# Kernel optimization log

Hardware: AMD Instinct MI355X
Metric: run time of the kernel (lower is better)

Reference implementation:

```python
import jax, jax.numpy as jnp
import numpy as np

# config
HIDDEN = 1024
NUM_EXPERTS = 16
TOP_K = 4
MOE_INTER = 512
NUM_SHARED = 2
SHARED_INTER = MOE_INTER * NUM_SHARED  # 1024
NORM_TOPK = True
ROUTED_SCALE = 1.0
NUM_TOKENS = 1024


def setup_inputs() -> dict:
    key = jax.random.key(0)
    ks = jax.random.split(key, 8)
    s = 0.02
    return {
        "hidden_states": jax.random.normal(ks[0], (NUM_TOKENS, HIDDEN), jnp.float32),
        # router (BailingMoEGate): weight [E, H], no bias
        "router_w": jax.random.normal(ks[1], (NUM_EXPERTS, HIDDEN), jnp.float32) * s,
        # routed experts: gate/up proj [E, H, I], down proj [E, I, H]
        "w_gate": jax.random.normal(ks[2], (NUM_EXPERTS, HIDDEN, MOE_INTER), jnp.float32) * s,
        "w_up": jax.random.normal(ks[3], (NUM_EXPERTS, HIDDEN, MOE_INTER), jnp.float32) * s,
        "w_down": jax.random.normal(ks[4], (NUM_EXPERTS, MOE_INTER, HIDDEN), jnp.float32) * s,
        # shared experts (BailingMoEMLP, merged gate_up): [H, 2*Is], [Is, H]
        "ws_gate_up": jax.random.normal(ks[5], (HIDDEN, 2 * SHARED_INTER), jnp.float32) * s,
        "ws_down": jax.random.normal(ks[6], (SHARED_INTER, HIDDEN), jnp.float32) * s,
    }


def _moe_forward(x, router_w, w_gate, w_up, w_down, ws_gate_up, ws_down):
    T = x.shape[0]
    # ---- router: logits -> softmax -> top-k (score_function='softmax', no bias)
    logits = jnp.einsum("th,eh->te", x, router_w)          # [T, E]
    probs = jax.nn.softmax(logits, axis=-1)
    topk_w, topk_idx = jax.lax.top_k(probs, TOP_K)         # [T, K]
    if NORM_TOPK:
        topk_w = topk_w / jnp.sum(topk_w, axis=-1, keepdims=True)
    topk_w = topk_w * ROUTED_SCALE
    # sparse combine weights [T, E] (zeros for non-selected experts)
    combine = jnp.zeros((T, NUM_EXPERTS), x.dtype).at[
        jnp.arange(T)[:, None], topk_idx
    ].set(topk_w.astype(x.dtype))
    # ---- routed experts: SiLU(x W_gate) * (x W_up) then W_down, weighted combine
    g = jnp.einsum("th,ehi->tei", x, w_gate)               # [T, E, I]
    u = jnp.einsum("th,ehi->tei", x, w_up)
    h = jax.nn.silu(g) * u
    routed = jnp.einsum("tei,eih,te->th", h, w_down, combine)
    # ---- shared experts (dense SwiGLU MLP)
    gu = x @ ws_gate_up                                    # [T, 2*Is]
    g_s, u_s = jnp.split(gu, 2, axis=-1)
    shared = (jax.nn.silu(g_s) * u_s) @ ws_down
    return routed + shared


def reference(hidden_states, router_w, w_gate, w_up, w_down, ws_gate_up, ws_down):
    return _moe_forward(hidden_states, router_w, w_gate, w_up, w_down,
                        ws_gate_up, ws_down)
```

## Files before the change

### kernel.cpp

```cpp
#include <hip/hip_runtime.h>
#include <stdint.h>


typedef __attribute__((ext_vector_type(8))) unsigned short ushort8;
typedef __attribute__((ext_vector_type(4))) float f32x4;
typedef __attribute__((ext_vector_type(8))) __bf16 bf16x8;

#define T_TOK 1024
#define HID   1024
#define NEXP  16
#define TOPK  4
#define MINTER 512
#define SINTER 1024

constexpr size_t WGU_E = 32 * 1024 * 32;
constexpr size_t WD_E  = 16 * 1024 * 32;

constexpr size_t OFF_COUNTS = 0;
constexpr size_t OFF_LIST   = 1024;
constexpr size_t OFF_WT     = OFF_LIST  + 65536;
constexpr size_t OFF_TIDX   = OFF_WT    + 65536;
constexpr size_t OFF_XB     = OFF_TIDX  + 65536;
constexpr size_t OFF_HR     = OFF_XB    + 2097152;
constexpr size_t OFF_HS     = OFF_HR    + 4194304;
constexpr size_t OFF_WGU    = OFF_HS    + 2097152;
constexpr size_t OFF_WD     = OFF_WGU   + 33554432;
constexpr size_t OFF_WSGU   = OFF_WD    + 16777216;
constexpr size_t OFF_WSD    = OFF_WSGU  + 4194304;
constexpr size_t OFF_ROUT   = OFF_WGU;

__device__ __forceinline__ unsigned short f2bf(float f) {
  union { float f; uint32_t u; } v; v.f = f;
  uint32_t r = (v.u + 0x7FFFu + ((v.u >> 16) & 1u)) >> 16;
  return (unsigned short)r;
}
__device__ __forceinline__ float bfu2f(uint32_t u) {
  union { uint32_t u; float f; } v; v.u = u << 16; return v.f;
}
__device__ __forceinline__ bf16x8 as_bf16x8(ushort8 s) {
  union { ushort8 s; bf16x8 b; } u; u.s = s; return u.b;
}
__device__ __forceinline__ float silu(float g) { return g / (1.f + __expf(-g)); }

__device__ __forceinline__ void glds16(const unsigned short* g, unsigned short* l) {
  __builtin_amdgcn_global_load_lds(
      (const __attribute__((address_space(1))) unsigned int*)g,
      (__attribute__((address_space(3))) unsigned int*)l, 16, 0, 0);
}

#define PIPE_BARRIER4() asm volatile("s_waitcnt vmcnt(4) lgkmcnt(0)\ns_barrier" ::: "memory")
#define PIPE_BARRIER0() asm volatile("s_waitcnt vmcnt(0) lgkmcnt(0)\ns_barrier" ::: "memory")

__global__ void init_kernel(int* counts) {
  if (threadIdx.x < NEXP) counts[threadIdx.x] = 0;
}

__global__ __launch_bounds__(64) void router_kernel(
    const float* __restrict__ x, const float* __restrict__ rw,
    int* counts, int* list, float* wt, int* tIdx,
    unsigned short* __restrict__ Xb) {
  const int t = blockIdx.x, l = threadIdx.x;
  float xv[16];
#pragma unroll
  for (int j = 0; j < 16; j++) xv[j] = x[t * HID + j * 64 + l];
#pragma unroll
  for (int j = 0; j < 16; j++) Xb[t * HID + j * 64 + l] = f2bf(xv[j]);
  float p[NEXP];
#pragma unroll
  for (int e = 0; e < NEXP; e++) {
    float s = 0.f;
#pragma unroll
    for (int j = 0; j < 16; j++) s += xv[j] * rw[e * HID + j * 64 + l];
#pragma unroll
    for (int off = 32; off > 0; off >>= 1) s += __shfl_xor(s, off);
    p[e] = s;
  }
  float mx = p[0];
#pragma unroll
  for (int e = 1; e < NEXP; e++) mx = fmaxf(mx, p[e]);
  int idx[TOPK]; float w4[TOPK]; float wsum = 0.f; unsigned used = 0u;
#pragma unroll
  for (int k = 0; k < TOPK; k++) {
    float bv = -1e30f; int bi = 0;
#pragma unroll
    for (int e = 0; e < NEXP; e++)
      if (!((used >> e) & 1u) && p[e] > bv) { bv = p[e]; bi = e; }
    used |= 1u << bi;
    idx[k] = bi;
    w4[k] = __expf(p[bi] - mx);
    wsum += w4[k];
  }
  const float inv = 1.f / wsum;
  if (l < TOPK) {
    const int e = idx[l];
    const int pos = atomicAdd(&counts[e], 1);
    list[e * 1024 + pos] = t;
    wt[e * 1024 + pos]   = w4[l] * inv;
    tIdx[t * TOPK + l]   = (e << 10) | pos;
  }
}

__global__ __launch_bounds__(256) void pack_all_kernel(
    const float* __restrict__ Wg, const float* __restrict__ Wu,
    const float* __restrict__ Wd, const float* __restrict__ Wsgu,
    const float* __restrict__ Wsd,
    unsigned short* __restrict__ WGUp, unsigned short* __restrict__ WDp,
    unsigned short* __restrict__ WSGUp, unsigned short* __restrict__ WSDp) {
  const int bid = blockIdx.x;
  const float* src; unsigned short* dst; int C, Nj, kp0, r0, c0, jbase, ilv;
  if (bid < 2048) {
    const int e = bid >> 7, loc = bid & 127, kt = loc >> 3, nt = loc & 7;
    src = Wg + (size_t)e * HID * MINTER; dst = WGUp + (size_t)e * WGU_E;
    C = MINTER; Nj = 1024; kp0 = 2 * kt; r0 = 64 * kt; c0 = 64 * nt;
    jbase = 128 * nt; ilv = 1;
  } else if (bid < 4096) {
    const int e = (bid - 2048) >> 7, loc = bid & 127, kt = loc >> 3, nt = loc & 7;
    src = Wu + (size_t)e * HID * MINTER; dst = WGUp + (size_t)e * WGU_E;
    C = MINTER; Nj = 1024; kp0 = 2 * kt; r0 = 64 * kt; c0 = 64 * nt;
    jbase = 128 * nt + 16; ilv = 1;
  } else if (bid < 6144) {
    const int e = (bid - 4096) >> 7, loc = bid & 127, kt = loc >> 4, nt = loc & 15;
    src = Wd + (size_t)e * MINTER * HID; dst = WDp + (size_t)e * WD_E;
    C = HID; Nj = 1024; kp0 = 2 * kt; r0 = 64 * kt; c0 = 64 * nt;
    jbase = 64 * nt; ilv = 0;
  } else if (bid < 6656) {
    const int loc = bid - 6144, kt = loc >> 5, nt = loc & 31;
    src = Wsgu; dst = WSGUp;
    C = 2048; Nj = 2048; kp0 = 2 * kt; r0 = 64 * kt; c0 = 64 * nt;
    const int isU = (nt >= 16), ntc = nt & 15;
    jbase = 128 * ntc + 16 * isU; ilv = 1;
  } else {
    const int loc = bid - 6656, kt = loc >> 4, nt = loc & 15;
    src = Wsd; dst = WSDp;
    C = HID; Nj = 1024; kp0 = 2 * kt; r0 = 64 * kt; c0 = 64 * nt;
    jbase = 64 * nt; ilv = 0;
  }
  __shared__ float tile[64][65];
  const int t = threadIdx.x;
  {
    const int r = t >> 4, c4 = (t & 15) * 4;
#pragma unroll
    for (int p = 0; p < 4; p++) {
      const int rr = p * 16 + r;
      const float4 v = *(const float4*)(src + (size_t)(r0 + rr) * C + c0 + c4);
      tile[rr][c4 + 0] = v.x; tile[rr][c4 + 1] = v.y;
      tile[rr][c4 + 2] = v.z; tile[rr][c4 + 3] = v.w;
    }
  }
  __syncthreads();
  {
    const int n = t >> 2, k8 = (t & 3) * 8;
    const int j = jbase + (ilv ? (32 * (n >> 4) + (n & 15)) : n);
#pragma unroll
    for (int h = 0; h < 2; h++) {
      const int k = 32 * h + k8;
      union { unsigned short u[8]; ushort8 v; } pk;
#pragma unroll
      for (int i = 0; i < 8; i++) pk.u[i] = f2bf(tile[k + i][n]);
      *(ushort8*)(dst + ((size_t)(kp0 + h) * Nj + j) * 32 + k8) = pk.v;
    }
  }
}

__global__ __launch_bounds__(256, 3) void phase1_kernel(
    const unsigned short* __restrict__ Xb,
    const unsigned short* __restrict__ WGUp,
    const unsigned short* __restrict__ WSGUp,
    const int* __restrict__ counts, const int* __restrict__ list,
    const float* __restrict__ wt,
    unsigned short* __restrict__ Hr,
    unsigned short* __restrict__ Hs) {
  const int z = blockIdx.z, x = blockIdx.x, y = blockIdx.y;
  const bool routed = (z < NEXP);
  int cnt = 0, base = 0;
  if (routed) {
    if (x >= 8) return;
    cnt = counts[z];
    if (y * 128 >= cnt) return;
#pragma unroll
    for (int i = 0; i < NEXP; i++) base += (i < z) ? counts[i] : 0;
  }
  __shared__ __align__(16) unsigned short sA[3][128 * 32];
  __shared__ __align__(16) unsigned short sB[3][128 * 32];
  const int tid = threadIdx.x, w = tid >> 6, l = tid & 63;
  const int wm = w >> 1, wn = w & 1, m0 = y * 128;
  const int swz = ((l & 3) ^ ((l >> 3) & 3)) * 8;
  const int Nj = routed ? 1024 : 2048;

  const unsigned short* aS[2];
#pragma unroll
  for (int ii = 0; ii < 2; ii++) {
    const int r = 32 * w + 16 * ii + (l >> 2);
    const unsigned short* row = routed
        ? Xb + (size_t)list[z * 1024 + min(m0 + r, cnt - 1)] * HID
        : Xb + (size_t)(m0 + r) * HID;
    aS[ii] = row + swz;
  }
  const unsigned short* pan = routed ? WGUp + (size_t)z * WGU_E : WSGUp;
  const unsigned short* bS[2];
#pragma unroll
  for (int ii = 0; ii < 2; ii++)
    bS[ii] = pan + ((size_t)(x * 128 + 32 * w + 16 * ii + (l >> 2))) * 32 + swz;
  const size_t bStep = (size_t)Nj * 32;

  const int rsw = ((l >> 4) ^ (((l & 15) >> 1) & 3)) * 8;
  int aOff[4], bOff[4];
#pragma unroll
  for (int i = 0; i < 4; i++) aOff[i] = (64 * wm + 16 * i + (l & 15)) * 32 + rsw;
#pragma unroll
  for (int jt = 0; jt < 4; jt++) bOff[jt] = (64 * wn + 16 * jt + (l & 15)) * 32 + rsw;

  f32x4 acc[4][4];
#pragma unroll
  for (int i = 0; i < 4; i++)
#pragma unroll
    for (int jt = 0; jt < 4; jt++) acc[i][jt] = (f32x4){0.f, 0.f, 0.f, 0.f};

  auto stage = [&](int s, int b) {
    glds16(aS[0] + s * 32, &sA[b][(32 * w) * 32]);
    glds16(aS[1] + s * 32, &sA[b][(32 * w + 16) * 32]);
    glds16(bS[0] + s * bStep, &sB[b][(32 * w) * 32]);
    glds16(bS[1] + s * bStep, &sB[b][(32 * w + 16) * 32]);
  };

  const int steps = HID / 32;
  stage(0, 0); stage(1, 1);
#pragma unroll 1
  for (int s = 0; s < steps; s++) {
    const int cb = s % 3;
    if (s + 2 < steps)      { PIPE_BARRIER4(); stage(s + 2, (s + 2) % 3); }
    else if (s + 1 < steps) { PIPE_BARRIER4(); }
    else                    { PIPE_BARRIER0(); }
    const unsigned short* A = &sA[cb][0];
    const unsigned short* B = &sB[cb][0];
    bf16x8 af[4], bfr[4];
#pragma unroll
    for (int i = 0; i < 4; i++) af[i] = as_bf16x8(*(const ushort8*)(A + aOff[i]));
#pragma unroll
    for (int jt = 0; jt < 4; jt++) bfr[jt] = as_bf16x8(*(const ushort8*)(B + bOff[jt]));
#pragma unroll
    for (int jt = 0; jt < 4; jt++)
#pragma unroll
      for (int i = 0; i < 4; i++)
        acc[i][jt] = __builtin_amdgcn_mfma_f32_16x16x32_bf16(af[i], bfr[jt], acc[i][jt], 0, 0, 0);
  }

  const int rl = (l >> 4) * 4, cl = l & 15;
  const int panel = 2 * x + wn;
#pragma unroll
  for (int i = 0; i < 4; i++)
#pragma unroll
    for (int r = 0; r < 4; r++) {
      const int grow = m0 + 64 * wm + 16 * i + rl + r;
#pragma unroll
      for (int p = 0; p < 2; p++) {
        const float g = acc[i][2 * p][r], u = acc[i][2 * p + 1][r];
        if (routed) {
          if (grow < cnt) {
            const float h = silu(g) * u * wt[z * 1024 + grow];
            Hr[((size_t)panel * 4096 + base + grow) * 32 + 16 * p + cl] = f2bf(h);
          }
        } else {
          const float h = silu(g) * u;
          Hs[((size_t)panel * 1024 + grow) * 32 + 16 * p + cl] = f2bf(h);
        }
      }
    }
}

__global__ __launch_bounds__(256, 3) void phase2_kernel(
    const unsigned short* __restrict__ Hr, const unsigned short* __restrict__ Hs,
    const unsigned short* __restrict__ WDp, const unsigned short* __restrict__ WSDp,
    const int* __restrict__ counts,
    unsigned short* __restrict__ Rout,
    float* __restrict__ out) {
  const int z = blockIdx.z, x = blockIdx.x, y = blockIdx.y;
  const bool routed = (z < NEXP);
  int cnt = 0, base = 0, steps;
  if (routed) {
    cnt = counts[z];
    if (y * 128 >= cnt) return;
#pragma unroll
    for (int i = 0; i < NEXP; i++) base += (i < z) ? counts[i] : 0;
    steps = MINTER / 32;
  } else {
    steps = SINTER / 32;
  }
  __shared__ __align__(16) unsigned short sA[3][128 * 32];
  __shared__ __align__(16) unsigned short sB[3][128 * 32];
  const int tid = threadIdx.x, w = tid >> 6, l = tid & 63;
  const int wm = w >> 1, wn = w & 1, m0 = y * 128;
  const int swz = ((l & 3) ^ ((l >> 3) & 3)) * 8;
  const size_t aStep = (size_t)(routed ? 4096 : 1024) * 32;

  const unsigned short* aS[2];
#pragma unroll
  for (int ii = 0; ii < 2; ii++) {
    const int r = 32 * w + 16 * ii + (l >> 2);
    const int R = routed ? (base + min(m0 + r, cnt - 1)) : (m0 + r);
    aS[ii] = (routed ? Hr : Hs) + (size_t)R * 32 + swz;
  }
  const unsigned short* pan = routed ? WDp + (size_t)z * WD_E : WSDp;
  const unsigned short* bS[2];
#pragma unroll
  for (int ii = 0; ii < 2; ii++)
    bS[ii] = pan + ((size_t)(x * 128 + 32 * w + 16 * ii + (l >> 2))) * 32 + swz;
  const size_t bStep = (size_t)1024 * 32;

  const int rsw = ((l >> 4) ^ (((l & 15) >> 1) & 3)) * 8;
  int aOff[4], bOff[4];
#pragma unroll
  for (int i = 0; i < 4; i++) aOff[i] = (64 * wm + 16 * i + (l & 15)) * 32 + rsw;
#pragma unroll
  for (int jt = 0; jt < 4; jt++) bOff[jt] = (64 * wn + 16 * jt + (l & 15)) * 32 + rsw;

  f32x4 acc[4][4];
#pragma unroll
  for (int i = 0; i < 4; i++)
#pragma unroll
    for (int jt = 0; jt < 4; jt++) acc[i][jt] = (f32x4){0.f, 0.f, 0.f, 0.f};

  auto stage = [&](int s, int b) {
    glds16(aS[0] + s * aStep, &sA[b][(32 * w) * 32]);
    glds16(aS[1] + s * aStep, &sA[b][(32 * w + 16) * 32]);
    glds16(bS[0] + s * bStep, &sB[b][(32 * w) * 32]);
    glds16(bS[1] + s * bStep, &sB[b][(32 * w + 16) * 32]);
  };

  stage(0, 0); stage(1, 1);
#pragma unroll 1
  for (int s = 0; s < steps; s++) {
    const int cb = s % 3;
    if (s + 2 < steps)      { PIPE_BARRIER4(); stage(s + 2, (s + 2) % 3); }
    else if (s + 1 < steps) { PIPE_BARRIER4(); }
    else                    { PIPE_BARRIER0(); }
    const unsigned short* A = &sA[cb][0];
    const unsigned short* B = &sB[cb][0];
    bf16x8 af[4], bfr[4];
#pragma unroll
    for (int i = 0; i < 4; i++) af[i] = as_bf16x8(*(const ushort8*)(A + aOff[i]));
#pragma unroll
    for (int jt = 0; jt < 4; jt++) bfr[jt] = as_bf16x8(*(const ushort8*)(B + bOff[jt]));
#pragma unroll
    for (int jt = 0; jt < 4; jt++)
#pragma unroll
      for (int i = 0; i < 4; i++)
        acc[i][jt] = __builtin_amdgcn_mfma_f32_16x16x32_bf16(af[i], bfr[jt], acc[i][jt], 0, 0, 0);
  }

  const int rl = (l >> 4) * 4, cl = l & 15;
#pragma unroll
  for (int i = 0; i < 4; i++)
#pragma unroll
    for (int r = 0; r < 4; r++) {
      const int grow = m0 + 64 * wm + 16 * i + rl + r;
#pragma unroll
      for (int jt = 0; jt < 4; jt++) {
        const int col = 128 * x + 64 * wn + 16 * jt + cl;
        if (routed) {
          if (grow < cnt)
            Rout[(size_t)(base + grow) * HID + col] = f2bf(acc[i][jt][r]);
        } else {
          out[(size_t)grow * HID + col] = acc[i][jt][r];
        }
      }
    }
}

__global__ __launch_bounds__(256) void combine_kernel(
    const unsigned short* __restrict__ Rout, const int* __restrict__ counts,
    const int* __restrict__ tIdx, float* __restrict__ out) {
  __shared__ int sb[NEXP];
  if (threadIdx.x == 0) {
    int s = 0;
#pragma unroll
    for (int e = 0; e < NEXP; e++) { sb[e] = s; s += counts[e]; }
  }
  __syncthreads();
  const int t = blockIdx.x, c4 = threadIdx.x * 4;
  float4 o = *(const float4*)(out + (size_t)t * HID + c4);
#pragma unroll
  for (int k = 0; k < TOPK; k++) {
    const int v = tIdx[t * TOPK + k];
    const int row = sb[v >> 10] + (v & 1023);
    const uint2 rv = *(const uint2*)(Rout + (size_t)row * HID + c4);
    o.x += bfu2f(rv.x & 0xffffu); o.y += bfu2f(rv.x >> 16);
    o.z += bfu2f(rv.y & 0xffffu); o.w += bfu2f(rv.y >> 16);
  }
  *(float4*)(out + (size_t)t * HID + c4) = o;
}

extern "C" void kernel_launch(void* const* d_in, const int* in_sizes, int n_in,
                              void* d_out, int out_size, void* d_ws, size_t ws_size,
                              hipStream_t stream) {
  const float* x      = (const float*)d_in[0];
  const float* rw     = (const float*)d_in[1];
  const float* w_gate = (const float*)d_in[2];
  const float* w_up   = (const float*)d_in[3];
  const float* w_down = (const float*)d_in[4];
  const float* ws_gu  = (const float*)d_in[5];
  const float* ws_dn  = (const float*)d_in[6];
  float* out = (float*)d_out;
  char* ws = (char*)d_ws;

  int*   counts = (int*)  (ws + OFF_COUNTS);
  int*   list   = (int*)  (ws + OFF_LIST);
  float* wtbuf  = (float*)(ws + OFF_WT);
  int*   tIdx   = (int*)  (ws + OFF_TIDX);
  unsigned short* Xb    = (unsigned short*)(ws + OFF_XB);
  unsigned short* Hr    = (unsigned short*)(ws + OFF_HR);
  unsigned short* Hs    = (unsigned short*)(ws + OFF_HS);
  unsigned short* WGUp  = (unsigned short*)(ws + OFF_WGU);
  unsigned short* WDp   = (unsigned short*)(ws + OFF_WD);
  unsigned short* WSGUp = (unsigned short*)(ws + OFF_WSGU);
  unsigned short* WSDp  = (unsigned short*)(ws + OFF_WSD);
  unsigned short* Rout  = (unsigned short*)(ws + OFF_ROUT);

  init_kernel<<<1, 64, 0, stream>>>(counts);
  router_kernel<<<T_TOK, 64, 0, stream>>>(x, rw, counts, list, wtbuf, tIdx, Xb);
  pack_all_kernel<<<6912, 256, 0, stream>>>(
      w_gate, w_up, w_down, ws_gu, ws_dn, WGUp, WDp, WSGUp, WSDp);
  phase1_kernel<<<dim3(16, 8, 17), 256, 0, stream>>>(
      Xb, WGUp, WSGUp, counts, list, wtbuf, Hr, Hs);
  phase2_kernel<<<dim3(8, 8, 17), 256, 0, stream>>>(
      Hr, Hs, WDp, WSDp, counts, Rout, out);
  combine_kernel<<<T_TOK, 256, 0, stream>>>(Rout, counts, tIdx, out);
  (void)in_sizes; (void)n_in; (void)out_size; (void)ws_size;
}
```

Baseline: 249.1 us.

## Drop weight pre-pack pass; load fp32 weights directly and convert in-GEMM

```diff
diff --git a/kernel.cpp b/kernel.cpp
--- a/kernel.cpp
+++ b/kernel.cpp
@@ -12,9 +12,6 @@
 #define TOPK  4
 #define MINTER 512
 #define SINTER 1024
-
-constexpr size_t WGU_E = 32 * 1024 * 32;
-constexpr size_t WD_E  = 16 * 1024 * 32;
 
 constexpr size_t OFF_COUNTS = 0;
 constexpr size_t OFF_LIST   = 1024;
@@ -23,11 +20,7 @@
 constexpr size_t OFF_XB     = OFF_TIDX  + 65536;
 constexpr size_t OFF_HR     = OFF_XB    + 2097152;
 constexpr size_t OFF_HS     = OFF_HR    + 4194304;
-constexpr size_t OFF_WGU    = OFF_HS    + 2097152;
-constexpr size_t OFF_WD     = OFF_WGU   + 33554432;
-constexpr size_t OFF_WSGU   = OFF_WD    + 16777216;
-constexpr size_t OFF_WSD    = OFF_WSGU  + 4194304;
-constexpr size_t OFF_ROUT   = OFF_WGU;
+constexpr size_t OFF_ROUT   = OFF_HS    + 2097152;
 
 __device__ __forceinline__ unsigned short f2bf(float f) {
   union { float f; uint32_t u; } v; v.f = f;
@@ -40,6 +33,10 @@
 __device__ __forceinline__ bf16x8 as_bf16x8(ushort8 s) {
   union { ushort8 s; bf16x8 b; } u; u.s = s; return u.b;
 }
+__device__ __forceinline__ uint32_t pk2(float hi, float lo) {
+  union { float f; uint32_t u; } a, b; a.f = hi; b.f = lo;
+  return ((a.u + 0x8000u) & 0xFFFF0000u) | ((b.u + 0x8000u) >> 16);
+}
 __device__ __forceinline__ float silu(float g) { return g / (1.f + __expf(-g)); }
 
 __device__ __forceinline__ void glds16(const unsigned short* g, unsigned short* l) {
@@ -48,8 +45,9 @@
       (__attribute__((address_space(3))) unsigned int*)l, 16, 0, 0);
 }
 
-#define PIPE_BARRIER4() asm volatile("s_waitcnt vmcnt(4) lgkmcnt(0)\ns_barrier" ::: "memory")
-#define PIPE_BARRIER0() asm volatile("s_waitcnt vmcnt(0) lgkmcnt(0)\ns_barrier" ::: "memory")
+#define WAIT_VM4() asm volatile("s_waitcnt vmcnt(4)" ::: "memory")
+#define WAIT_VM0() asm volatile("s_waitcnt vmcnt(0)" ::: "memory")
+#define BAR_LGKM() asm volatile("s_waitcnt lgkmcnt(0)\ns_barrier" ::: "memory")
 
 __global__ void init_kernel(int* counts) {
   if (threadIdx.x < NEXP) counts[threadIdx.x] = 0;
@@ -100,115 +98,67 @@
   }
 }
 
-__global__ __launch_bounds__(256) void pack_all_kernel(
-    const float* __restrict__ Wg, const float* __restrict__ Wu,
-    const float* __restrict__ Wd, const float* __restrict__ Wsgu,
-    const float* __restrict__ Wsd,
-    unsigned short* __restrict__ WGUp, unsigned short* __restrict__ WDp,
-    unsigned short* __restrict__ WSGUp, unsigned short* __restrict__ WSDp) {
-  const int bid = blockIdx.x;
-  const float* src; unsigned short* dst; int C, Nj, kp0, r0, c0, jbase, ilv;
-  if (bid < 2048) {
-    const int e = bid >> 7, loc = bid & 127, kt = loc >> 3, nt = loc & 7;
-    src = Wg + (size_t)e * HID * MINTER; dst = WGUp + (size_t)e * WGU_E;
-    C = MINTER; Nj = 1024; kp0 = 2 * kt; r0 = 64 * kt; c0 = 64 * nt;
-    jbase = 128 * nt; ilv = 1;
-  } else if (bid < 4096) {
-    const int e = (bid - 2048) >> 7, loc = bid & 127, kt = loc >> 3, nt = loc & 7;
-    src = Wu + (size_t)e * HID * MINTER; dst = WGUp + (size_t)e * WGU_E;
-    C = MINTER; Nj = 1024; kp0 = 2 * kt; r0 = 64 * kt; c0 = 64 * nt;
-    jbase = 128 * nt + 16; ilv = 1;
-  } else if (bid < 6144) {
-    const int e = (bid - 4096) >> 7, loc = bid & 127, kt = loc >> 4, nt = loc & 15;
-    src = Wd + (size_t)e * MINTER * HID; dst = WDp + (size_t)e * WD_E;
-    C = HID; Nj = 1024; kp0 = 2 * kt; r0 = 64 * kt; c0 = 64 * nt;
-    jbase = 64 * nt; ilv = 0;
-  } else if (bid < 6656) {
-    const int loc = bid - 6144, kt = loc >> 5, nt = loc & 31;
-    src = Wsgu; dst = WSGUp;
-    C = 2048; Nj = 2048; kp0 = 2 * kt; r0 = 64 * kt; c0 = 64 * nt;
-    const int isU = (nt >= 16), ntc = nt & 15;
-    jbase = 128 * ntc + 16 * isU; ilv = 1;
-  } else {
-    const int loc = bid - 6656, kt = loc >> 4, nt = loc & 15;
-    src = Wsd; dst = WSDp;
-    C = HID; Nj = 1024; kp0 = 2 * kt; r0 = 64 * kt; c0 = 64 * nt;
-    jbase = 64 * nt; ilv = 0;
-  }
-  __shared__ float tile[64][65];
-  const int t = threadIdx.x;
-  {
-    const int r = t >> 4, c4 = (t & 15) * 4;
-#pragma unroll
-    for (int p = 0; p < 4; p++) {
-      const int rr = p * 16 + r;
-      const float4 v = *(const float4*)(src + (size_t)(r0 + rr) * C + c0 + c4);
-      tile[rr][c4 + 0] = v.x; tile[rr][c4 + 1] = v.y;
-      tile[rr][c4 + 2] = v.z; tile[rr][c4 + 3] = v.w;
-    }
-  }
-  __syncthreads();
-  {
-    const int n = t >> 2, k8 = (t & 3) * 8;
-    const int j = jbase + (ilv ? (32 * (n >> 4) + (n & 15)) : n);
-#pragma unroll
-    for (int h = 0; h < 2; h++) {
-      const int k = 32 * h + k8;
-      union { unsigned short u[8]; ushort8 v; } pk;
-#pragma unroll
-      for (int i = 0; i < 8; i++) pk.u[i] = f2bf(tile[k + i][n]);
-      *(ushort8*)(dst + ((size_t)(kp0 + h) * Nj + j) * 32 + k8) = pk.v;
-    }
-  }
-}
-
 __global__ __launch_bounds__(256, 3) void phase1_kernel(
     const unsigned short* __restrict__ Xb,
-    const unsigned short* __restrict__ WGUp,
-    const unsigned short* __restrict__ WSGUp,
+    const float* __restrict__ Wg, const float* __restrict__ Wu,
+    const float* __restrict__ Wsgu,
     const int* __restrict__ counts, const int* __restrict__ list,
     const float* __restrict__ wt,
     unsigned short* __restrict__ Hr,
     unsigned short* __restrict__ Hs) {
   const int z = blockIdx.z, x = blockIdx.x, y = blockIdx.y;
-  const bool routed = (z < NEXP);
+  const bool routed = (z > 0);
+  const int e = z - 1;
   int cnt = 0, base = 0;
   if (routed) {
     if (x >= 8) return;
-    cnt = counts[z];
+    cnt = counts[e];
     if (y * 128 >= cnt) return;
 #pragma unroll
-    for (int i = 0; i < NEXP; i++) base += (i < z) ? counts[i] : 0;
-  }
-  __shared__ __align__(16) unsigned short sA[3][128 * 32];
-  __shared__ __align__(16) unsigned short sB[3][128 * 32];
+    for (int i = 0; i < NEXP; i++) base += (i < e) ? counts[i] : 0;
+  }
+  __shared__ __align__(16) unsigned short sA[2][128 * 32];
+  __shared__ __align__(16) float sBF[2][32 * 132];
   const int tid = threadIdx.x, w = tid >> 6, l = tid & 63;
   const int wm = w >> 1, wn = w & 1, m0 = y * 128;
   const int swz = ((l & 3) ^ ((l >> 3) & 3)) * 8;
-  const int Nj = routed ? 1024 : 2048;
 
   const unsigned short* aS[2];
 #pragma unroll
   for (int ii = 0; ii < 2; ii++) {
     const int r = 32 * w + 16 * ii + (l >> 2);
     const unsigned short* row = routed
-        ? Xb + (size_t)list[z * 1024 + min(m0 + r, cnt - 1)] * HID
+        ? Xb + (size_t)list[e * 1024 + min(m0 + r, cnt - 1)] * HID
         : Xb + (size_t)(m0 + r) * HID;
     aS[ii] = row + swz;
   }
-  const unsigned short* pan = routed ? WGUp + (size_t)z * WGU_E : WSGUp;
-  const unsigned short* bS[2];
-#pragma unroll
-  for (int ii = 0; ii < 2; ii++)
-    bS[ii] = pan + ((size_t)(x * 128 + 32 * w + 16 * ii + (l >> 2))) * 32 + swz;
-  const size_t bStep = (size_t)Nj * 32;
+
+  const int kRow = 8 * w + (l >> 3);
+  const int cB = (l & 7) * 8;
+  const float* gG0; const float* gU0; size_t bStepF;
+  if (routed) {
+    gG0 = Wg + ((size_t)e * HID + kRow) * MINTER + 64 * x + cB;
+    gU0 = Wu + ((size_t)e * HID + kRow) * MINTER + 64 * x + cB;
+    bStepF = (size_t)32 * MINTER;
+  } else {
+    gG0 = Wsgu + (size_t)kRow * 2048 + 64 * x + cB;
+    gU0 = gG0 + 1024;
+    bStepF = (size_t)32 * 2048;
+  }
+  const int Xw = (w & 3) << 4;
+  const int JG = 32 * (cB >> 4) + (cB & 15);
+  const int wG = kRow * 132 + (JG ^ Xw);
+  const int wU = kRow * 132 + ((JG | 16) ^ Xw);
 
   const int rsw = ((l >> 4) ^ (((l & 15) >> 1) & 3)) * 8;
-  int aOff[4], bOff[4];
+  int aOff[4];
 #pragma unroll
   for (int i = 0; i < 4; i++) aOff[i] = (64 * wm + 16 * i + (l & 15)) * 32 + rsw;
-#pragma unroll
-  for (int jt = 0; jt < 4; jt++) bOff[jt] = (64 * wn + 16 * jt + (l & 15)) * 32 + rsw;
+  int bBase[4];
+#pragma unroll
+  for (int jt = 0; jt < 4; jt++)
+    bBase[jt] = (l >> 4) * (8 * 132) +
+                ((64 * wn + 16 * jt + (l & 15)) ^ ((l >> 4) << 4));
 
   f32x4 acc[4][4];
 #pragma unroll
@@ -216,33 +166,60 @@
 #pragma unroll
     for (int jt = 0; jt < 4; jt++) acc[i][jt] = (f32x4){0.f, 0.f, 0.f, 0.f};
 
-  auto stage = [&](int s, int b) {
-    glds16(aS[0] + s * 32, &sA[b][(32 * w) * 32]);
-    glds16(aS[1] + s * 32, &sA[b][(32 * w + 16) * 32]);
-    glds16(bS[0] + s * bStep, &sB[b][(32 * w) * 32]);
-    glds16(bS[1] + s * bStep, &sB[b][(32 * w + 16) * 32]);
+  float4 brA[4], brB[4];
+  auto loadB = [&](int s, float4* br) {
+    const float* g = gG0 + (size_t)s * bStepF;
+    const float* u = gU0 + (size_t)s * bStepF;
+    br[0] = *(const float4*)g; br[1] = *(const float4*)(g + 4);
+    br[2] = *(const float4*)u; br[3] = *(const float4*)(u + 4);
+  };
+  auto storeB = [&](int b, const float4* br) {
+    float* d = &sBF[b][0];
+    *(float4*)(d + wG) = br[0]; *(float4*)(d + wG + 4) = br[1];
+    *(float4*)(d + wU) = br[2]; *(float4*)(d + wU + 4) = br[3];
+  };
+  auto stageA = [&](int s, int b) {
+    glds16(aS[0] + (size_t)s * 32, &sA[b][(32 * w) * 32]);
+    glds16(aS[1] + (size_t)s * 32, &sA[b][(32 * w + 16) * 32]);
   };
 
   const int steps = HID / 32;
-  stage(0, 0); stage(1, 1);
+  stageA(0, 0);
+  loadB(0, brA);
+  loadB(1, brB);
+  WAIT_VM4();
+  storeB(0, brA);
+  BAR_LGKM();
+
+  auto stepf = [&](int s, float4* brFill, float4* brSt) {
+    const int cur = s & 1;
+    if (s + 1 < steps) stageA(s + 1, cur ^ 1);
+    if (s + 2 < steps) loadB(s + 2, brFill);
+    const unsigned short* A = &sA[cur][0];
+    const float* Bf = &sBF[cur][0];
+    bf16x8 af[4];
+#pragma unroll
+    for (int i = 0; i < 4; i++) af[i] = as_bf16x8(*(const ushort8*)(A + aOff[i]));
+#pragma unroll
+    for (int jt = 0; jt < 4; jt++) {
+      float f[8];
+#pragma unroll
+      for (int q = 0; q < 8; q++) f[q] = Bf[bBase[jt] + q * 132];
+      union { uint32_t u[4]; bf16x8 v; } qq;
+      qq.u[0] = pk2(f[1], f[0]); qq.u[1] = pk2(f[3], f[2]);
+      qq.u[2] = pk2(f[5], f[4]); qq.u[3] = pk2(f[7], f[6]);
+#pragma unroll
+      for (int i = 0; i < 4; i++)
+        acc[i][jt] = __builtin_amdgcn_mfma_f32_16x16x32_bf16(af[i], qq.v, acc[i][jt], 0, 0, 0);
+    }
+    if (s + 2 < steps) { WAIT_VM4(); } else { WAIT_VM0(); }
+    if (s + 1 < steps) storeB((s + 1) & 1, brSt);
+    BAR_LGKM();
+  };
 #pragma unroll 1
-  for (int s = 0; s < steps; s++) {
-    const int cb = s % 3;
-    if (s + 2 < steps)      { PIPE_BARRIER4(); stage(s + 2, (s + 2) % 3); }
-    else if (s + 1 < steps) { PIPE_BARRIER4(); }
-    else                    { PIPE_BARRIER0(); }
-    const unsigned short* A = &sA[cb][0];
-    const unsigned short* B = &sB[cb][0];
-    bf16x8 af[4], bfr[4];
-#pragma unroll
-    for (int i = 0; i < 4; i++) af[i] = as_bf16x8(*(const ushort8*)(A + aOff[i]));
-#pragma unroll
-    for (int jt = 0; jt < 4; jt++) bfr[jt] = as_bf16x8(*(const ushort8*)(B + bOff[jt]));
-#pragma unroll
-    for (int jt = 0; jt < 4; jt++)
-#pragma unroll
-      for (int i = 0; i < 4; i++)
-        acc[i][jt] = __builtin_amdgcn_mfma_f32_16x16x32_bf16(af[i], bfr[jt], acc[i][jt], 0, 0, 0);
+  for (int s = 0; s < steps; s += 2) {
+    stepf(s, brA, brB);
+    stepf(s + 1, brB, brA);
   }
 
   const int rl = (l >> 4) * 4, cl = l & 15;
@@ -257,7 +234,7 @@
         const float g = acc[i][2 * p][r], u = acc[i][2 * p + 1][r];
         if (routed) {
           if (grow < cnt) {
-            const float h = silu(g) * u * wt[z * 1024 + grow];
+            const float h = silu(g) * u * wt[e * 1024 + grow];
             Hr[((size_t)panel * 4096 + base + grow) * 32 + 16 * p + cl] = f2bf(h);
           }
         } else {
@@ -270,24 +247,25 @@
 
 __global__ __launch_bounds__(256, 3) void phase2_kernel(
     const unsigned short* __restrict__ Hr, const unsigned short* __restrict__ Hs,
-    const unsigned short* __restrict__ WDp, const unsigned short* __restrict__ WSDp,
+    const float* __restrict__ Wd, const float* __restrict__ Wsd,
     const int* __restrict__ counts,
     unsigned short* __restrict__ Rout,
     float* __restrict__ out) {
   const int z = blockIdx.z, x = blockIdx.x, y = blockIdx.y;
-  const bool routed = (z < NEXP);
+  const bool routed = (z > 0);
+  const int e = z - 1;
   int cnt = 0, base = 0, steps;
   if (routed) {
-    cnt = counts[z];
+    cnt = counts[e];
     if (y * 128 >= cnt) return;
 #pragma unroll
-    for (int i = 0; i < NEXP; i++) base += (i < z) ? counts[i] : 0;
+    for (int i = 0; i < NEXP; i++) base += (i < e) ? counts[i] : 0;
     steps = MINTER / 32;
   } else {
     steps = SINTER / 32;
   }
-  __shared__ __align__(16) unsigned short sA[3][128 * 32];
-  __shared__ __align__(16) unsigned short sB[3][128 * 32];
+  __shared__ __align__(16) unsigned short sA[2][128 * 32];
+  __shared__ __align__(16) float sBF[2][32 * 132];
   const int tid = threadIdx.x, w = tid >> 6, l = tid & 63;
   const int wm = w >> 1, wn = w & 1, m0 = y * 128;
   const int swz = ((l & 3) ^ ((l >> 3) & 3)) * 8;
@@ -300,19 +278,26 @@
     const int R = routed ? (base + min(m0 + r, cnt - 1)) : (m0 + r);
     aS[ii] = (routed ? Hr : Hs) + (size_t)R * 32 + swz;
   }
-  const unsigned short* pan = routed ? WDp + (size_t)z * WD_E : WSDp;
-  const unsigned short* bS[2];
-#pragma unroll
-  for (int ii = 0; ii < 2; ii++)
-    bS[ii] = pan + ((size_t)(x * 128 + 32 * w + 16 * ii + (l >> 2))) * 32 + swz;
-  const size_t bStep = (size_t)1024 * 32;
+
+  const int kRow = 8 * w + (l >> 3);
+  const int cB = (l & 7) * 16;
+  const float* gB0 = routed
+      ? Wd + ((size_t)e * MINTER + kRow) * HID + 128 * x + cB
+      : Wsd + (size_t)kRow * HID + 128 * x + cB;
+  const size_t bStepF = (size_t)32 * HID;
+
+  const int Xw = (w & 3) << 4;
+  const int wB = kRow * 132 + (cB ^ Xw);
 
   const int rsw = ((l >> 4) ^ (((l & 15) >> 1) & 3)) * 8;
-  int aOff[4], bOff[4];
+  int aOff[4];
 #pragma unroll
   for (int i = 0; i < 4; i++) aOff[i] = (64 * wm + 16 * i + (l & 15)) * 32 + rsw;
-#pragma unroll
-  for (int jt = 0; jt < 4; jt++) bOff[jt] = (64 * wn + 16 * jt + (l & 15)) * 32 + rsw;
+  int bBase[4];
+#pragma unroll
+  for (int jt = 0; jt < 4; jt++)
+    bBase[jt] = (l >> 4) * (8 * 132) +
+                ((64 * wn + 16 * jt + (l & 15)) ^ ((l >> 4) << 4));
 
   f32x4 acc[4][4];
 #pragma unroll
@@ -320,32 +305,58 @@
 #pragma unroll
     for (int jt = 0; jt < 4; jt++) acc[i][jt] = (f32x4){0.f, 0.f, 0.f, 0.f};
 
-  auto stage = [&](int s, int b) {
-    glds16(aS[0] + s * aStep, &sA[b][(32 * w) * 32]);
-    glds16(aS[1] + s * aStep, &sA[b][(32 * w + 16) * 32]);
-    glds16(bS[0] + s * bStep, &sB[b][(32 * w) * 32]);
-    glds16(bS[1] + s * bStep, &sB[b][(32 * w + 16) * 32]);
-  };
-
-  stage(0, 0); stage(1, 1);
+  float4 brA[4], brB[4];
+  auto loadB = [&](int s, float4* br) {
+    const float* g = gB0 + (size_t)s * bStepF;
+    br[0] = *(const float4*)g;       br[1] = *(const float4*)(g + 4);
+    br[2] = *(const float4*)(g + 8); br[3] = *(const float4*)(g + 12);
+  };
+  auto storeB = [&](int b, const float4* br) {
+    float* d = &sBF[b][0];
+    *(float4*)(d + wB) = br[0];     *(float4*)(d + wB + 4) = br[1];
+    *(float4*)(d + wB + 8) = br[2]; *(float4*)(d + wB + 12) = br[3];
+  };
+  auto stageA = [&](int s, int b) {
+    glds16(aS[0] + (size_t)s * aStep, &sA[b][(32 * w) * 32]);
+    glds16(aS[1] + (size_t)s * aStep, &sA[b][(32 * w + 16) * 32]);
+  };
+
+  stageA(0, 0);
+  loadB(0, brA);
+  loadB(1, brB);
+  WAIT_VM4();
+  storeB(0, brA);
+  BAR_LGKM();
+
+  auto stepf = [&](int s, float4* brFill, float4* brSt) {
+    const int cur = s & 1;
+    if (s + 1 < steps) stageA(s + 1, cur ^ 1);
+    if (s + 2 < steps) loadB(s + 2, brFill);
+    const unsigned short* A = &sA[cur][0];
+    const float* Bf = &sBF[cur][0];
+    bf16x8 af[4];
+#pragma unroll
+    for (int i = 0; i < 4; i++) af[i] = as_bf16x8(*(const ushort8*)(A + aOff[i]));
+#pragma unroll
+    for (int jt = 0; jt < 4; jt++) {
+      float f[8];
+#pragma unroll
+      for (int q = 0; q < 8; q++) f[q] = Bf[bBase[jt] + q * 132];
+      union { uint32_t u[4]; bf16x8 v; } qq;
+      qq.u[0] = pk2(f[1], f[0]); qq.u[1] = pk2(f[3], f[2]);
+      qq.u[2] = pk2(f[5], f[4]); qq.u[3] = pk2(f[7], f[6]);
+#pragma unroll
+      for (int i = 0; i < 4; i++)
+        acc[i][jt] = __builtin_amdgcn_mfma_f32_16x16x32_bf16(af[i], qq.v, acc[i][jt], 0, 0, 0);
+    }
+    if (s + 2 < steps) { WAIT_VM4(); } else { WAIT_VM0(); }
+    if (s + 1 < steps) storeB((s + 1) & 1, brSt);
+    BAR_LGKM();
+  };
 #pragma unroll 1
-  for (int s = 0; s < steps; s++) {
-    const int cb = s % 3;
-    if (s + 2 < steps)      { PIPE_BARRIER4(); stage(s + 2, (s + 2) % 3); }
-    else if (s + 1 < steps) { PIPE_BARRIER4(); }
-    else                    { PIPE_BARRIER0(); }
-    const unsigned short* A = &sA[cb][0];
-    const unsigned short* B = &sB[cb][0];
-    bf16x8 af[4], bfr[4];
-#pragma unroll
-    for (int i = 0; i < 4; i++) af[i] = as_bf16x8(*(const ushort8*)(A + aOff[i]));
-#pragma unroll
-    for (int jt = 0; jt < 4; jt++) bfr[jt] = as_bf16x8(*(const ushort8*)(B + bOff[jt]));
-#pragma unroll
-    for (int jt = 0; jt < 4; jt++)
-#pragma unroll
-      for (int i = 0; i < 4; i++)
-        acc[i][jt] = __builtin_amdgcn_mfma_f32_16x16x32_bf16(af[i], bfr[jt], acc[i][jt], 0, 0, 0);
+  for (int s = 0; s < steps; s += 2) {
+    stepf(s, brA, brB);
+    stepf(s + 1, brB, brA);
   }
 
   const int rl = (l >> 4) * 4, cl = l & 15;
@@ -407,23 +418,17 @@
   int*   list   = (int*)  (ws + OFF_LIST);
   float* wtbuf  = (float*)(ws + OFF_WT);
   int*   tIdx   = (int*)  (ws + OFF_TIDX);
-  unsigned short* Xb    = (unsigned short*)(ws + OFF_XB);
-  unsigned short* Hr    = (unsigned short*)(ws + OFF_HR);
-  unsigned short* Hs    = (unsigned short*)(ws + OFF_HS);
-  unsigned short* WGUp  = (unsigned short*)(ws + OFF_WGU);
-  unsigned short* WDp   = (unsigned short*)(ws + OFF_WD);
-  unsigned short* WSGUp = (unsigned short*)(ws + OFF_WSGU);
-  unsigned short* WSDp  = (unsigned short*)(ws + OFF_WSD);
-  unsigned short* Rout  = (unsigned short*)(ws + OFF_ROUT);
+  unsigned short* Xb   = (unsigned short*)(ws + OFF_XB);
+  unsigned short* Hr   = (unsigned short*)(ws + OFF_HR);
+  unsigned short* Hs   = (unsigned short*)(ws + OFF_HS);
+  unsigned short* Rout = (unsigned short*)(ws + OFF_ROUT);
 
   init_kernel<<<1, 64, 0, stream>>>(counts);
   router_kernel<<<T_TOK, 64, 0, stream>>>(x, rw, counts, list, wtbuf, tIdx, Xb);
-  pack_all_kernel<<<6912, 256, 0, stream>>>(
-      w_gate, w_up, w_down, ws_gu, ws_dn, WGUp, WDp, WSGUp, WSDp);
   phase1_kernel<<<dim3(16, 8, 17), 256, 0, stream>>>(
-      Xb, WGUp, WSGUp, counts, list, wtbuf, Hr, Hs);
+      Xb, w_gate, w_up, ws_gu, counts, list, wtbuf, Hr, Hs);
   phase2_kernel<<<dim3(8, 8, 17), 256, 0, stream>>>(
-      Hr, Hs, WDp, WSDp, counts, Rout, out);
+      Hr, Hs, w_down, ws_dn, counts, Rout, out);
   combine_kernel<<<T_TOK, 256, 0, stream>>>(Rout, counts, tIdx, out);
   (void)in_sizes; (void)n_in; (void)out_size; (void)ws_size;
 }
```

Result: slower. 414.1 us (+66.3%).

## Replace combine kernel with atomic scatter-add and use double-buffered pipeline

Applied to the files above, without the earlier changes.

```diff
diff --git a/kernel.cpp b/kernel.cpp
--- a/kernel.cpp
+++ b/kernel.cpp
@@ -19,24 +19,19 @@
 constexpr size_t OFF_COUNTS = 0;
 constexpr size_t OFF_LIST   = 1024;
 constexpr size_t OFF_WT     = OFF_LIST  + 65536;
-constexpr size_t OFF_TIDX   = OFF_WT    + 65536;
-constexpr size_t OFF_XB     = OFF_TIDX  + 65536;
+constexpr size_t OFF_XB     = OFF_WT    + 65536;
 constexpr size_t OFF_HR     = OFF_XB    + 2097152;
 constexpr size_t OFF_HS     = OFF_HR    + 4194304;
 constexpr size_t OFF_WGU    = OFF_HS    + 2097152;
 constexpr size_t OFF_WD     = OFF_WGU   + 33554432;
 constexpr size_t OFF_WSGU   = OFF_WD    + 16777216;
 constexpr size_t OFF_WSD    = OFF_WSGU  + 4194304;
-constexpr size_t OFF_ROUT   = OFF_WGU;
 
 __device__ __forceinline__ unsigned short f2bf(float f) {
   union { float f; uint32_t u; } v; v.f = f;
   uint32_t r = (v.u + 0x7FFFu + ((v.u >> 16) & 1u)) >> 16;
   return (unsigned short)r;
 }
-__device__ __forceinline__ float bfu2f(uint32_t u) {
-  union { uint32_t u; float f; } v; v.u = u << 16; return v.f;
-}
 __device__ __forceinline__ bf16x8 as_bf16x8(ushort8 s) {
   union { ushort8 s; bf16x8 b; } u; u.s = s; return u.b;
 }
@@ -48,16 +43,17 @@
       (__attribute__((address_space(3))) unsigned int*)l, 16, 0, 0);
 }
 
-#define PIPE_BARRIER4() asm volatile("s_waitcnt vmcnt(4) lgkmcnt(0)\ns_barrier" ::: "memory")
 #define PIPE_BARRIER0() asm volatile("s_waitcnt vmcnt(0) lgkmcnt(0)\ns_barrier" ::: "memory")
 
-__global__ void init_kernel(int* counts) {
-  if (threadIdx.x < NEXP) counts[threadIdx.x] = 0;
+__global__ __launch_bounds__(256) void init_kernel(int* counts, float* out) {
+  if (blockIdx.x == 0 && threadIdx.x < NEXP) counts[threadIdx.x] = 0;
+  const size_t t = (size_t)blockIdx.x * 256 + threadIdx.x;
+  *(float4*)(out + t * 4) = (float4){0.f, 0.f, 0.f, 0.f};
 }
 
 __global__ __launch_bounds__(64) void router_kernel(
     const float* __restrict__ x, const float* __restrict__ rw,
-    int* counts, int* list, float* wt, int* tIdx,
+    int* counts, int* list, float* wt,
     unsigned short* __restrict__ Xb) {
   const int t = blockIdx.x, l = threadIdx.x;
   float xv[16];
@@ -96,7 +92,6 @@
     const int pos = atomicAdd(&counts[e], 1);
     list[e * 1024 + pos] = t;
     wt[e * 1024 + pos]   = w4[l] * inv;
-    tIdx[t * TOPK + l]   = (e << 10) | pos;
   }
 }
 
@@ -162,7 +157,7 @@
   }
 }
 
-__global__ __launch_bounds__(256, 3) void phase1_kernel(
+__global__ __launch_bounds__(256, 5) void phase1_kernel(
     const unsigned short* __restrict__ Xb,
     const unsigned short* __restrict__ WGUp,
     const unsigned short* __restrict__ WSGUp,
@@ -171,17 +166,18 @@
     unsigned short* __restrict__ Hr,
     unsigned short* __restrict__ Hs) {
   const int z = blockIdx.z, x = blockIdx.x, y = blockIdx.y;
-  const bool routed = (z < NEXP);
+  const bool routed = (z > 0);
+  const int e = z - 1;
   int cnt = 0, base = 0;
   if (routed) {
     if (x >= 8) return;
-    cnt = counts[z];
+    cnt = counts[e];
     if (y * 128 >= cnt) return;
 #pragma unroll
-    for (int i = 0; i < NEXP; i++) base += (i < z) ? counts[i] : 0;
-  }
-  __shared__ __align__(16) unsigned short sA[3][128 * 32];
-  __shared__ __align__(16) unsigned short sB[3][128 * 32];
+    for (int i = 0; i < NEXP; i++) base += (i < e) ? counts[i] : 0;
+  }
+  __shared__ __align__(16) unsigned short sA[2][128 * 32];
+  __shared__ __align__(16) unsigned short sB[2][128 * 32];
   const int tid = threadIdx.x, w = tid >> 6, l = tid & 63;
   const int wm = w >> 1, wn = w & 1, m0 = y * 128;
   const int swz = ((l & 3) ^ ((l >> 3) & 3)) * 8;
@@ -192,11 +188,11 @@
   for (int ii = 0; ii < 2; ii++) {
     const int r = 32 * w + 16 * ii + (l >> 2);
     const unsigned short* row = routed
-        ? Xb + (size_t)list[z * 1024 + min(m0 + r, cnt - 1)] * HID
+        ? Xb + (size_t)list[e * 1024 + min(m0 + r, cnt - 1)] * HID
         : Xb + (size_t)(m0 + r) * HID;
     aS[ii] = row + swz;
   }
-  const unsigned short* pan = routed ? WGUp + (size_t)z * WGU_E : WSGUp;
+  const unsigned short* pan = routed ? WGUp + (size_t)e * WGU_E : WSGUp;
   const unsigned short* bS[2];
 #pragma unroll
   for (int ii = 0; ii < 2; ii++)
@@ -217,22 +213,21 @@
     for (int jt = 0; jt < 4; jt++) acc[i][jt] = (f32x4){0.f, 0.f, 0.f, 0.f};
 
   auto stage = [&](int s, int b) {
-    glds16(aS[0] + s * 32, &sA[b][(32 * w) * 32]);
-    glds16(aS[1] + s * 32, &sA[b][(32 * w + 16) * 32]);
-    glds16(bS[0] + s * bStep, &sB[b][(32 * w) * 32]);
-    glds16(bS[1] + s * bStep, &sB[b][(32 * w + 16) * 32]);
+    glds16(aS[0] + (size_t)s * 32, &sA[b][(32 * w) * 32]);
+    glds16(aS[1] + (size_t)s * 32, &sA[b][(32 * w + 16) * 32]);
+    glds16(bS[0] + (size_t)s * bStep, &sB[b][(32 * w) * 32]);
+    glds16(bS[1] + (size_t)s * bStep, &sB[b][(32 * w + 16) * 32]);
   };
 
   const int steps = HID / 32;
-  stage(0, 0); stage(1, 1);
+  stage(0, 0);
+  PIPE_BARRIER0();
 #pragma unroll 1
   for (int s = 0; s < steps; s++) {
-    const int cb = s % 3;
-    if (s + 2 < steps)      { PIPE_BARRIER4(); stage(s + 2, (s + 2) % 3); }
-    else if (s + 1 < steps) { PIPE_BARRIER4(); }
-    else                    { PIPE_BARRIER0(); }
-    const unsigned short* A = &sA[cb][0];
-    const unsigned short* B = &sB[cb][0];
+    const int cur = s & 1;
+    if (s + 1 < steps) stage(s + 1, cur ^ 1);
+    const unsigned short* A = &sA[cur][0];
+    const unsigned short* B = &sB[cur][0];
     bf16x8 af[4], bfr[4];
 #pragma unroll
     for (int i = 0; i < 4; i++) af[i] = as_bf16x8(*(const ushort8*)(A + aOff[i]));
@@ -243,6 +238,7 @@
 #pragma unroll
       for (int i = 0; i < 4; i++)
         acc[i][jt] = __builtin_amdgcn_mfma_f32_16x16x32_bf16(af[i], bfr[jt], acc[i][jt], 0, 0, 0);
+    PIPE_BARRIER0();
   }
 
   const int rl = (l >> 4) * 4, cl = l & 15;
@@ -257,7 +253,7 @@
         const float g = acc[i][2 * p][r], u = acc[i][2 * p + 1][r];
         if (routed) {
           if (grow < cnt) {
-            const float h = silu(g) * u * wt[z * 1024 + grow];
+            const float h = silu(g) * u * wt[e * 1024 + grow];
             Hr[((size_t)panel * 4096 + base + grow) * 32 + 16 * p + cl] = f2bf(h);
           }
         } else {
@@ -268,26 +264,26 @@
     }
 }
 
-__global__ __launch_bounds__(256, 3) void phase2_kernel(
+__global__ __launch_bounds__(256, 5) void phase2_kernel(
     const unsigned short* __restrict__ Hr, const unsigned short* __restrict__ Hs,
     const unsigned short* __restrict__ WDp, const unsigned short* __restrict__ WSDp,
-    const int* __restrict__ counts,
-    unsigned short* __restrict__ Rout,
+    const int* __restrict__ counts, const int* __restrict__ list,
     float* __restrict__ out) {
   const int z = blockIdx.z, x = blockIdx.x, y = blockIdx.y;
-  const bool routed = (z < NEXP);
+  const bool routed = (z > 0);
+  const int e = z - 1;
   int cnt = 0, base = 0, steps;
   if (routed) {
-    cnt = counts[z];
+    cnt = counts[e];
     if (y * 128 >= cnt) return;
 #pragma unroll
-    for (int i = 0; i < NEXP; i++) base += (i < z) ? counts[i] : 0;
+    for (int i = 0; i < NEXP; i++) base += (i < e) ? counts[i] : 0;
     steps = MINTER / 32;
   } else {
     steps = SINTER / 32;
   }
-  __shared__ __align__(16) unsigned short sA[3][128 * 32];
-  __shared__ __align__(16) unsigned short sB[3][128 * 32];
+  __shared__ __align__(16) unsigned short sA[2][128 * 32];
+  __shared__ __align__(16) unsigned short sB[2][128 * 32];
   const int tid = threadIdx.x, w = tid >> 6, l = tid & 63;
   const int wm = w >> 1, wn = w & 1, m0 = y * 128;
   const int swz = ((l & 3) ^ ((l >> 3) & 3)) * 8;
@@ -300,7 +296,7 @@
     const int R = routed ? (base + min(m0 + r, cnt - 1)) : (m0 + r);
     aS[ii] = (routed ? Hr : Hs) + (size_t)R * 32 + swz;
   }
-  const unsigned short* pan = routed ? WDp + (size_t)z * WD_E : WSDp;
+  const unsigned short* pan = routed ? WDp + (size_t)e * WD_E : WSDp;
   const unsigned short* bS[2];
 #pragma unroll
   for (int ii = 0; ii < 2; ii++)
@@ -321,21 +317,20 @@
     for (int jt = 0; jt < 4; jt++) acc[i][jt] = (f32x4){0.f, 0.f, 0.f, 0.f};
 
   auto stage = [&](int s, int b) {
-    glds16(aS[0] + s * aStep, &sA[b][(32 * w) * 32]);
-    glds16(aS[1] + s * aStep, &sA[b][(32 * w + 16) * 32]);
-    glds16(bS[0] + s * bStep, &sB[b][(32 * w) * 32]);
-    glds16(bS[1] + s * bStep, &sB[b][(32 * w + 16) * 32]);
+    glds16(aS[0] + (size_t)s * aStep, &sA[b][(32 * w) * 32]);
+    glds16(aS[1] + (size_t)s * aStep, &sA[b][(32 * w + 16) * 32]);
+    glds16(bS[0] + (size_t)s * bStep, &sB[b][(32 * w) * 32]);
+    glds16(bS[1] + (size_t)s * bStep, &sB[b][(32 * w + 16) * 32]);
   };
 
-  stage(0, 0); stage(1, 1);
+  stage(0, 0);
+  PIPE_BARRIER0();
 #pragma unroll 1
   for (int s = 0; s < steps; s++) {
-    const int cb = s % 3;
-    if (s + 2 < steps)      { PIPE_BARRIER4(); stage(s + 2, (s + 2) % 3); }
-    else if (s + 1 < steps) { PIPE_BARRIER4(); }
-    else                    { PIPE_BARRIER0(); }
-    const unsigned short* A = &sA[cb][0];
-    const unsigned short* B = &sB[cb][0];
+    const int cur = s & 1;
+    if (s + 1 < steps) stage(s + 1, cur ^ 1);
+    const unsigned short* A = &sA[cur][0];
+    const unsigned short* B = &sB[cur][0];
     bf16x8 af[4], bfr[4];
 #pragma unroll
     for (int i = 0; i < 4; i++) af[i] = as_bf16x8(*(const ushort8*)(A + aOff[i]));
@@ -346,6 +341,7 @@
 #pragma unroll
       for (int i = 0; i < 4; i++)
         acc[i][jt] = __builtin_amdgcn_mfma_f32_16x16x32_bf16(af[i], bfr[jt], acc[i][jt], 0, 0, 0);
+    PIPE_BARRIER0();
   }
 
   const int rl = (l >> 4) * 4, cl = l & 15;
@@ -354,40 +350,14 @@
 #pragma unroll
     for (int r = 0; r < 4; r++) {
       const int grow = m0 + 64 * wm + 16 * i + rl + r;
+      if (routed && grow >= cnt) continue;
+      const int orow = routed ? list[e * 1024 + grow] : grow;
 #pragma unroll
       for (int jt = 0; jt < 4; jt++) {
         const int col = 128 * x + 64 * wn + 16 * jt + cl;
-        if (routed) {
-          if (grow < cnt)
-            Rout[(size_t)(base + grow) * HID + col] = f2bf(acc[i][jt][r]);
-        } else {
-          out[(size_t)grow * HID + col] = acc[i][jt][r];
-        }
+        atomicAdd(&out[(size_t)orow * HID + col], acc[i][jt][r]);
       }
     }
-}
-
-__global__ __launch_bounds__(256) void combine_kernel(
-    const unsigned short* __restrict__ Rout, const int* __restrict__ counts,
-    const int* __restrict__ tIdx, float* __restrict__ out) {
-  __shared__ int sb[NEXP];
-  if (threadIdx.x == 0) {
-    int s = 0;
-#pragma unroll
-    for (int e = 0; e < NEXP; e++) { sb[e] = s; s += counts[e]; }
-  }
-  __syncthreads();
-  const int t = blockIdx.x, c4 = threadIdx.x * 4;
-  float4 o = *(const float4*)(out + (size_t)t * HID + c4);
-#pragma unroll
-  for (int k = 0; k < TOPK; k++) {
-    const int v = tIdx[t * TOPK + k];
-    const int row = sb[v >> 10] + (v & 1023);
-    const uint2 rv = *(const uint2*)(Rout + (size_t)row * HID + c4);
-    o.x += bfu2f(rv.x & 0xffffu); o.y += bfu2f(rv.x >> 16);
-    o.z += bfu2f(rv.y & 0xffffu); o.w += bfu2f(rv.y >> 16);
-  }
-  *(float4*)(out + (size_t)t * HID + c4) = o;
 }
 
 extern "C" void kernel_launch(void* const* d_in, const int* in_sizes, int n_in,
@@ -406,7 +376,6 @@
   int*   counts = (int*)  (ws + OFF_COUNTS);
   int*   list   = (int*)  (ws + OFF_LIST);
   float* wtbuf  = (float*)(ws + OFF_WT);
-  int*   tIdx   = (int*)  (ws + OFF_TIDX);
   unsigned short* Xb    = (unsigned short*)(ws + OFF_XB);
   unsigned short* Hr    = (unsigned short*)(ws + OFF_HR);
   unsigned short* Hs    = (unsigned short*)(ws + OFF_HS);
@@ -414,16 +383,14 @@
   unsigned short* WDp   = (unsigned short*)(ws + OFF_WD);
   unsigned short* WSGUp = (unsigned short*)(ws + OFF_WSGU);
   unsigned short* WSDp  = (unsigned short*)(ws + OFF_WSD);
-  unsigned short* Rout  = (unsigned short*)(ws + OFF_ROUT);
-
-  init_kernel<<<1, 64, 0, stream>>>(counts);
-  router_kernel<<<T_TOK, 64, 0, stream>>>(x, rw, counts, list, wtbuf, tIdx, Xb);
+
+  init_kernel<<<1024, 256, 0, stream>>>(counts, out);
+  router_kernel<<<T_TOK, 64, 0, stream>>>(x, rw, counts, list, wtbuf, Xb);
   pack_all_kernel<<<6912, 256, 0, stream>>>(
       w_gate, w_up, w_down, ws_gu, ws_dn, WGUp, WDp, WSGUp, WSDp);
   phase1_kernel<<<dim3(16, 8, 17), 256, 0, stream>>>(
       Xb, WGUp, WSGUp, counts, list, wtbuf, Hr, Hs);
   phase2_kernel<<<dim3(8, 8, 17), 256, 0, stream>>>(
-      Hr, Hs, WDp, WSDp, counts, Rout, out);
-  combine_kernel<<<T_TOK, 256, 0, stream>>>(Rout, counts, tIdx, out);
+      Hr, Hs, WDp, WSDp, counts, list, out);
   (void)in_sizes; (void)n_in; (void)out_size; (void)ws_size;
 }
```

Result: slower. 299.4 us (+20.2%).
